# Performance work log

Hardware: AMD Instinct MI355X
Metric: run time of the kernel (lower is better)

## Reference

```python
import jax, jax.numpy as jnp
import numpy as np

MARGIN = 0.1
NUM_BINS = 1600  # FastAP histogram bins over squared-distance range [0, 4]


def _fastap_rewards(x, labels):
    """Per-query FastAP (Cakir et al.) with soft (triangular) histogram binning.
    x: [n, d] L2-normalized embeddings; labels: [n] int. Returns [n] rewards.
    Uses the fact that a triangular pulse of width delta spreads each distance
    over exactly two adjacent bins -> scatter-add instead of an [n,n,L] tensor."""
    n = x.shape[0]
    L = NUM_BINS + 1
    delta = 4.0 / NUM_BINS
    dist2 = jnp.clip(2.0 - 2.0 * (x @ x.T), 0.0, 4.0)  # [n, n]
    same = labels[:, None] == labels[None, :]
    eye = jnp.eye(n, dtype=bool)
    i_pos = same & ~eye
    i_neg = ~same

    t = dist2 / delta
    idx0 = jnp.clip(jnp.floor(t).astype(jnp.int32), 0, L - 1)
    idx1 = jnp.clip(idx0 + 1, 0, L - 1)
    frac = t - jnp.floor(t)
    rows = jnp.broadcast_to(jnp.arange(n)[:, None], (n, n))

    def hist(mask):
        m = mask.astype(x.dtype)
        h = jnp.zeros((n, L), x.dtype)
        h = h.at[rows, idx0].add((1.0 - frac) * m)
        h = h.at[rows, idx1].add(frac * m)
        return h

    h_pos = hist(i_pos)
    h_neg = hist(i_neg)
    H_pos = jnp.cumsum(h_pos, axis=1)
    H_all = jnp.cumsum(h_pos + h_neg, axis=1)
    n_pos = jnp.sum(i_pos, axis=1).astype(x.dtype)
    safe = H_all > 0
    ap = jnp.sum(jnp.where(safe, h_pos * H_pos / jnp.where(safe, H_all, 1.0), 0.0), axis=1)
    return jnp.where(n_pos > 0, ap / jnp.maximum(n_pos, 1.0), 0.0)


def _per_row_loss(inputs_col, targets_col, inputs_row, targets_row):
    """Vectorized form of compute_loss_list. Sorting in the original only serves
    to extract max pos / max neg similarity, so per-row maxima + masked sums
    reproduce the exact same math."""
    n = inputs_col.shape[0]
    sim = inputs_col @ inputs_row.T  # [n, m]
    pos = targets_col[:, None] == targets_row[None, :]
    neg = ~pos  # computed BEFORE removing the diagonal, as in the original
    eye = jnp.eye(n, dtype=bool)
    pos = pos.at[:, :n].set(pos[:, :n] & ~eye)

    has_pos = jnp.any(pos, axis=1)
    neg_max = jnp.max(jnp.where(neg, sim, -jnp.inf), axis=1)  # neg_pair_[-1]
    pos_max = jnp.max(jnp.where(pos, sim, -jnp.inf), axis=1)  # pos_pair_[-1]

    pos_sel = pos & (sim < (neg_max + MARGIN)[:, None])
    pos_loss = jnp.sum(jnp.where(pos_sel, 1.0 - sim, 0.0), axis=1)

    thr = jnp.maximum(0.6, pos_max) - MARGIN
    neg_sel = neg & (sim > thr[:, None])
    neg_loss = jnp.sum(jnp.where(neg_sel, sim, 0.0), axis=1)

    return jnp.where(has_pos, pos_loss + neg_loss, 0.0), n


def setup_inputs() -> dict:
    key = jax.random.key(0)
    k1, k2, k3, k4, k5 = jax.random.split(key, 5)
    n, m, d, ncls = 4096, 4096, 128, 512

    def unit(k, shape):
        v = jax.random.normal(k, shape, dtype=jnp.float32)
        return v / jnp.linalg.norm(v, axis=-1, keepdims=True)

    return {
        "inputs_col": unit(k1, (n, d)),
        "targets_col": jax.random.randint(k2, (n,), 0, ncls),
        "inputs_row": unit(k3, (m, d)),
        "targets_row": jax.random.randint(k4, (m,), 0, ncls),
        "reward_labels": jax.random.randint(k5, (n,), 0, ncls),
    }


def reference(inputs_col, targets_col, inputs_row, targets_row, reward_labels):
    loss_i, n = _per_row_loss(inputs_col, targets_col, inputs_row, targets_row)
    # torch.tensor(rewards) detaches rewards from the graph -> stop_gradient
    rewards = jax.lax.stop_gradient(_fastap_rewards(inputs_col, reward_labels))
    return jnp.sum(loss_i * (1.0 - rewards)) / n
```

## Files before the change

kernel.cpp:

```cpp
#include <hip/hip_runtime.h>


#define N_ROWS 4096
#define DIM 128
#define TILE 128
#define L_BINS 1601
#define WSCALE 65536.0f

typedef __bf16 bf16x8 __attribute__((ext_vector_type(8)));
typedef float f32x4 __attribute__((ext_vector_type(4)));

__device__ __forceinline__ unsigned short f32_to_bf16(float f) {
    unsigned int u = __float_as_uint(f);
    u = (u + 0x7FFFu + ((u >> 16) & 1u)) >> 16;
    return (unsigned short)u;
}

__device__ __forceinline__ float bf16_lo(unsigned int u) {
    return __uint_as_float(u << 16);
}
__device__ __forceinline__ float bf16_hi(unsigned int u) {
    return __uint_as_float(u & 0xFFFF0000u);
}

__device__ __forceinline__ void async_copy16(const void* g, void* l) {
    __builtin_amdgcn_global_load_lds(
        (const __attribute__((address_space(1))) unsigned int*)g,
        (__attribute__((address_space(3))) unsigned int*)l, 16, 0, 0);
}

__global__ __launch_bounds__(256) void cvt_bf16_kernel(const float* __restrict__ in,
                                                       unsigned short* __restrict__ out,
                                                       int count) {
    for (int idx = blockIdx.x * 256 + threadIdx.x; idx < count; idx += gridDim.x * 256)
        out[idx] = f32_to_bf16(in[idx]);
}

__global__ __launch_bounds__(256) void gemm_tile_kernel(const unsigned short* __restrict__ A,
                                                        const unsigned short* __restrict__ B,
                                                        unsigned short* __restrict__ C,
                                                        int N) {
    __shared__ unsigned short As[TILE * DIM];
    __shared__ unsigned short Bs[TILE * DIM];
    int w = threadIdx.x >> 6;
    int lane = threadIdx.x & 63;
    int tm = blockIdx.y, tn = blockIdx.x;

    const char* ga = (const char*)(A + (size_t)tm * TILE * DIM);
    const char* gb = (const char*)(B + (size_t)tn * TILE * DIM);
#pragma unroll
    for (int it = 0; it < 8; ++it) {
        int off = (w * 8 + it) * 1024;
        async_copy16(ga + off + lane * 16, (char*)As + off);
        async_copy16(gb + off + lane * 16, (char*)Bs + off);
    }
    __syncthreads();

    int wm = (w & 1) * 64;
    int wn = (w >> 1) * 64;
    int quad = lane >> 4;
    int l15 = lane & 15;

    f32x4 acc[4][4] = {};
#pragma unroll
    for (int kk = 0; kk < 4; ++kk) {
        int kb = kk * 32 + quad * 8;
        bf16x8 af[4], bfr[4];
#pragma unroll
        for (int mi = 0; mi < 4; ++mi)
            af[mi] = *(const bf16x8*)&As[(wm + mi * 16 + l15) * DIM + kb];
#pragma unroll
        for (int ni = 0; ni < 4; ++ni)
            bfr[ni] = *(const bf16x8*)&Bs[(wn + ni * 16 + l15) * DIM + kb];
#pragma unroll
        for (int mi = 0; mi < 4; ++mi)
#pragma unroll
            for (int ni = 0; ni < 4; ++ni)
                acc[mi][ni] = __builtin_amdgcn_mfma_f32_16x16x32_bf16(af[mi], bfr[ni], acc[mi][ni], 0, 0, 0);
    }

#pragma unroll
    for (int mi = 0; mi < 4; ++mi) {
        int row0 = tm * TILE + wm + mi * 16 + quad * 4;
#pragma unroll
        for (int ni = 0; ni < 4; ++ni) {
            int col = tn * TILE + wn + ni * 16 + l15;
#pragma unroll
            for (int r = 0; r < 4; ++r)
                C[(size_t)(row0 + r) * N + col] = f32_to_bf16(acc[mi][ni][r]);
        }
    }
}

__global__ __launch_bounds__(256) void loss_kernel(const unsigned short* __restrict__ sim,
                                                   const int* __restrict__ tcol,
                                                   const int* __restrict__ trow,
                                                   float* __restrict__ loss,
                                                   int n, int m) {
    __shared__ float ssim[N_ROWS];
    __shared__ char smask[N_ROWS];
    __shared__ float r1[256], r2[256];
    const float NEG_INF = -__builtin_huge_valf();
    int i = blockIdx.x;
    int t = threadIdx.x;
    int myt = tcol[i];

    const uint4* simv = (const uint4*)(sim + (size_t)i * m);
    const int4* labv = (const int4*)trow;

    float pmax = NEG_INF, nmax = NEG_INF;
    for (int v = t; v < (m >> 3); v += 256) {
        uint4 pk = simv[v];
        int4 l0 = labv[v * 2];
        int4 l1 = labv[v * 2 + 1];
        int j0 = v << 3;
        float s[8];
        s[0] = bf16_lo(pk.x); s[1] = bf16_hi(pk.x);
        s[2] = bf16_lo(pk.y); s[3] = bf16_hi(pk.y);
        s[4] = bf16_lo(pk.z); s[5] = bf16_hi(pk.z);
        s[6] = bf16_lo(pk.w); s[7] = bf16_hi(pk.w);
        int lab[8] = {l0.x, l0.y, l0.z, l0.w, l1.x, l1.y, l1.z, l1.w};
#pragma unroll
        for (int k = 0; k < 8; ++k) {
            int j = j0 + k;
            bool same = (lab[k] == myt);
            ssim[j] = s[k];
            smask[j] = same ? 1 : 0;
            if (same) {
                if (j != i && s[k] > pmax) pmax = s[k];
            } else {
                if (s[k] > nmax) nmax = s[k];
            }
        }
    }
    r1[t] = pmax; r2[t] = nmax;
    __syncthreads();
    for (int off = 128; off > 0; off >>= 1) {
        if (t < off) { r1[t] = fmaxf(r1[t], r1[t + off]); r2[t] = fmaxf(r2[t], r2[t + off]); }
        __syncthreads();
    }
    float pm = r1[0], nm = r2[0];
    __syncthreads();

    float thr_n = nm + 0.1f;
    float thr_p = fmaxf(0.6f, pm) - 0.1f;
    float pl = 0.f, nl = 0.f;
    for (int j = t; j < m; j += 256) {
        float s = ssim[j];
        if (smask[j]) {
            if (j != i && s < thr_n) pl += 1.f - s;
        } else {
            if (s > thr_p) nl += s;
        }
    }
    r1[t] = pl; r2[t] = nl;
    __syncthreads();
    for (int off = 128; off > 0; off >>= 1) {
        if (t < off) { r1[t] += r1[t + off]; r2[t] += r2[t + off]; }
        __syncthreads();
    }
    if (t == 0) loss[i] = (pm > NEG_INF) ? (r1[0] + r2[0]) : 0.f;
}

__global__ __launch_bounds__(256) void fastap_kernel(const unsigned short* __restrict__ gram,
                                                     const int* __restrict__ labels,
                                                     float* __restrict__ reward,
                                                     int n) {
    __shared__ unsigned int h_pos[L_BINS];
    __shared__ unsigned int h_all[L_BINS];
    __shared__ unsigned int sp[256], sa[256];
    __shared__ float fr[256];
    __shared__ int ir[256];
    int i = blockIdx.x;
    int t = threadIdx.x;

    for (int b = t; b < L_BINS; b += 256) { h_pos[b] = 0u; h_all[b] = 0u; }
    __syncthreads();

    int li = labels[i];
    int npos = 0;
    const uint4* gv = (const uint4*)(gram + (size_t)i * n);
    const int4* labv = (const int4*)labels;

    for (int v = t; v < (n >> 3); v += 256) {
        uint4 pk = gv[v];
        int4 l0 = labv[v * 2];
        int4 l1 = labv[v * 2 + 1];
        int j0 = v << 3;
        float s[8];
        s[0] = bf16_lo(pk.x); s[1] = bf16_hi(pk.x);
        s[2] = bf16_lo(pk.y); s[3] = bf16_hi(pk.y);
        s[4] = bf16_lo(pk.z); s[5] = bf16_hi(pk.z);
        s[6] = bf16_lo(pk.w); s[7] = bf16_hi(pk.w);
        int lab[8] = {l0.x, l0.y, l0.z, l0.w, l1.x, l1.y, l1.z, l1.w};
#pragma unroll
        for (int k = 0; k < 8; ++k) {
            int j = j0 + k;
            if (j == i) continue;
            float d2 = fminf(fmaxf(2.f - 2.f * s[k], 0.f), 4.f);
            float tt = d2 * 400.0f;
            float fl = floorf(tt);
            int i0 = (int)fl;
            if (i0 > L_BINS - 1) i0 = L_BINS - 1;
            int i1 = i0 + 1;
            if (i1 > L_BINS - 1) i1 = L_BINS - 1;
            unsigned int w1 = (unsigned int)((tt - fl) * WSCALE);
            unsigned int w0 = 65536u - w1;
            atomicAdd(&h_all[i0], w0);
            atomicAdd(&h_all[i1], w1);
            if (lab[k] == li) {
                atomicAdd(&h_pos[i0], w0);
                atomicAdd(&h_pos[i1], w1);
                npos++;
            }
        }
    }
    __syncthreads();

    const int CH = 7;
    int base = t * CH;
    unsigned int lp[CH], la[CH];
    unsigned int cp = 0u, ca = 0u;
    for (int k = 0; k < CH; ++k) {
        int idx = base + k;
        unsigned int hp = (idx < L_BINS) ? h_pos[idx] : 0u;
        unsigned int ha = (idx < L_BINS) ? h_all[idx] : 0u;
        cp += hp; ca += ha;
        lp[k] = cp; la[k] = ca;
    }
    sp[t] = cp; sa[t] = ca;
    __syncthreads();
    for (int off = 1; off < 256; off <<= 1) {
        unsigned int vp = 0u, va = 0u;
        if (t >= off) { vp = sp[t - off]; va = sa[t - off]; }
        __syncthreads();
        sp[t] += vp; sa[t] += va;
        __syncthreads();
    }
    unsigned int offp = sp[t] - cp, offa = sa[t] - ca;
    __syncthreads();

    float ap = 0.f;
    for (int k = 0; k < CH; ++k) {
        int idx = base + k;
        if (idx < L_BINS) {
            unsigned int hp = h_pos[idx];
            unsigned int Ha = la[k] + offa;
            if (hp > 0u && Ha > 0u) {
                float Hp = (float)(lp[k] + offp);
                ap += (float)hp * Hp / (float)Ha;
            }
        }
    }
    fr[t] = ap; ir[t] = npos;
    __syncthreads();
    for (int off = 128; off > 0; off >>= 1) {
        if (t < off) { fr[t] += fr[t + off]; ir[t] += ir[t + off]; }
        __syncthreads();
    }
    if (t == 0) {
        float np_ = (float)ir[0];
        reward[i] = (np_ > 0.f) ? fr[0] * (1.0f / WSCALE) / fmaxf(np_, 1.f) : 0.f;
    }
}

__global__ __launch_bounds__(256) void final_kernel(const float* __restrict__ loss,
                                                    const float* __restrict__ reward,
                                                    float* __restrict__ out, int n) {
    __shared__ float r[256];
    int t = threadIdx.x;
    float s = 0.f;
    for (int j = t; j < n; j += 256) s += loss[j] * (1.f - reward[j]);
    r[t] = s;
    __syncthreads();
    for (int off = 128; off > 0; off >>= 1) {
        if (t < off) r[t] += r[t + off];
        __syncthreads();
    }
    if (t == 0) out[0] = r[0] / (float)n;
}

extern "C" void kernel_launch(void* const* d_in, const int* in_sizes, int n_in,
                              void* d_out, int out_size, void* d_ws, size_t ws_size,
                              hipStream_t stream) {
    const float* inputs_col = (const float*)d_in[0];
    const int* targets_col = (const int*)d_in[1];
    const float* inputs_row = (const float*)d_in[2];
    const int* targets_row = (const int*)d_in[3];
    const int* reward_labels = (const int*)d_in[4];
    float* out = (float*)d_out;

    const int n = N_ROWS, m = N_ROWS, d = DIM;
    char* ws = (char*)d_ws;
    unsigned short* simbuf = (unsigned short*)ws;
    unsigned short* Abf = (unsigned short*)(ws + (size_t)33554432);
    unsigned short* Rbf = (unsigned short*)(ws + (size_t)33554432 + 1048576);
    float* loss = (float*)(ws + (size_t)33554432 + 2 * 1048576);
    float* reward = loss + n;

    cvt_bf16_kernel<<<2048, 256, 0, stream>>>(inputs_col, Abf, n * d);
    cvt_bf16_kernel<<<2048, 256, 0, stream>>>(inputs_row, Rbf, m * d);

    dim3 ggrid(n / TILE, n / TILE);
    gemm_tile_kernel<<<ggrid, 256, 0, stream>>>(Abf, Rbf, simbuf, m);

    loss_kernel<<<n, 256, 0, stream>>>(simbuf, targets_col, targets_row, loss, n, m);

    gemm_tile_kernel<<<ggrid, 256, 0, stream>>>(Abf, Abf, simbuf, n);

    fastap_kernel<<<n, 256, 0, stream>>>(simbuf, reward_labels, reward, n);

    final_kernel<<<1, 256, 0, stream>>>(loss, reward, out, n);
}
```

Measured before the change: 150.7 us.

## Merge conversions and GEMMs, use wave-per-row loss and packed 64-bit histogram

Fuses the two bf16 conversion launches into one vectorized kernel and runs both GEMMs in a single launch via a z grid dimension, writing to separate buffers. The loss kernel now uses one wavefront per row, keeps the data in registers and reduces with shuffles instead of shared memory and block barriers. The FastAP kernel packs the positive and all-pairs histograms into one 64-bit shared atomic per bin, which halves the atomics, and uses wave shuffles for the scan and reductions. The cost is a second 32MB similarity buffer and 64-bit LDS atomics.

```diff
diff --git a/kernel.cpp b/kernel.cpp
--- a/kernel.cpp
+++ b/kernel.cpp
@@ -5,7 +5,6 @@
 #define DIM 128
 #define TILE 128
 #define L_BINS 1601
-#define WSCALE 65536.0f
 
 typedef __bf16 bf16x8 __attribute__((ext_vector_type(8)));
 typedef float f32x4 __attribute__((ext_vector_type(4)));
@@ -23,28 +22,48 @@
     return __uint_as_float(u & 0xFFFF0000u);
 }
 
+__device__ __forceinline__ void unpack8(uint4 pk, float* s) {
+    s[0] = bf16_lo(pk.x); s[1] = bf16_hi(pk.x);
+    s[2] = bf16_lo(pk.y); s[3] = bf16_hi(pk.y);
+    s[4] = bf16_lo(pk.z); s[5] = bf16_hi(pk.z);
+    s[6] = bf16_lo(pk.w); s[7] = bf16_hi(pk.w);
+}
+
 __device__ __forceinline__ void async_copy16(const void* g, void* l) {
     __builtin_amdgcn_global_load_lds(
         (const __attribute__((address_space(1))) unsigned int*)g,
         (__attribute__((address_space(3))) unsigned int*)l, 16, 0, 0);
 }
 
-__global__ __launch_bounds__(256) void cvt_bf16_kernel(const float* __restrict__ in,
-                                                       unsigned short* __restrict__ out,
-                                                       int count) {
-    for (int idx = blockIdx.x * 256 + threadIdx.x; idx < count; idx += gridDim.x * 256)
-        out[idx] = f32_to_bf16(in[idx]);
+__global__ __launch_bounds__(256) void cvt2_kernel(const float4* __restrict__ a,
+                                                   const float4* __restrict__ b,
+                                                   ushort4* __restrict__ oa,
+                                                   ushort4* __restrict__ ob,
+                                                   int nvec) {
+    for (int idx = blockIdx.x * 256 + threadIdx.x; idx < 2 * nvec; idx += gridDim.x * 256) {
+        bool second = idx >= nvec;
+        int k = second ? idx - nvec : idx;
+        float4 v = second ? b[k] : a[k];
+        ushort4 o;
+        o.x = f32_to_bf16(v.x); o.y = f32_to_bf16(v.y);
+        o.z = f32_to_bf16(v.z); o.w = f32_to_bf16(v.w);
+        if (second) ob[k] = o; else oa[k] = o;
+    }
 }
 
 __global__ __launch_bounds__(256) void gemm_tile_kernel(const unsigned short* __restrict__ A,
-                                                        const unsigned short* __restrict__ B,
-                                                        unsigned short* __restrict__ C,
+                                                        const unsigned short* __restrict__ B0,
+                                                        const unsigned short* __restrict__ B1,
+                                                        unsigned short* __restrict__ C0,
+                                                        unsigned short* __restrict__ C1,
                                                         int N) {
     __shared__ unsigned short As[TILE * DIM];
     __shared__ unsigned short Bs[TILE * DIM];
     int w = threadIdx.x >> 6;
     int lane = threadIdx.x & 63;
     int tm = blockIdx.y, tn = blockIdx.x;
+    const unsigned short* B = blockIdx.z ? B1 : B0;
+    unsigned short* C = blockIdx.z ? C1 : C0;
 
     const char* ga = (const char*)(A + (size_t)tm * TILE * DIM);
     const char* gb = (const char*)(B + (size_t)tn * TILE * DIM);
@@ -97,84 +116,79 @@
                                                    const int* __restrict__ trow,
                                                    float* __restrict__ loss,
                                                    int n, int m) {
-    __shared__ float ssim[N_ROWS];
-    __shared__ char smask[N_ROWS];
-    __shared__ float r1[256], r2[256];
-    const float NEG_INF = -__builtin_huge_valf();
-    int i = blockIdx.x;
-    int t = threadIdx.x;
+    int i = (blockIdx.x * 256 + threadIdx.x) >> 6;
+    int lane = threadIdx.x & 63;
     int myt = tcol[i];
 
     const uint4* simv = (const uint4*)(sim + (size_t)i * m);
     const int4* labv = (const int4*)trow;
 
-    float pmax = NEG_INF, nmax = NEG_INF;
-    for (int v = t; v < (m >> 3); v += 256) {
-        uint4 pk = simv[v];
-        int4 l0 = labv[v * 2];
-        int4 l1 = labv[v * 2 + 1];
-        int j0 = v << 3;
+    uint4 pk[8];
+    unsigned long long posm = 0ull, negm = 0ull;
+    float pmax = -3e38f, nmax = -3e38f;
+#pragma unroll
+    for (int v = 0; v < 8; ++v) {
+        int vi = v * 64 + lane;
+        pk[v] = simv[vi];
+        int4 l0 = labv[2 * vi];
+        int4 l1 = labv[2 * vi + 1];
+        int j0 = vi * 8;
         float s[8];
-        s[0] = bf16_lo(pk.x); s[1] = bf16_hi(pk.x);
-        s[2] = bf16_lo(pk.y); s[3] = bf16_hi(pk.y);
-        s[4] = bf16_lo(pk.z); s[5] = bf16_hi(pk.z);
-        s[6] = bf16_lo(pk.w); s[7] = bf16_hi(pk.w);
+        unpack8(pk[v], s);
         int lab[8] = {l0.x, l0.y, l0.z, l0.w, l1.x, l1.y, l1.z, l1.w};
 #pragma unroll
         for (int k = 0; k < 8; ++k) {
             int j = j0 + k;
             bool same = (lab[k] == myt);
-            ssim[j] = s[k];
-            smask[j] = same ? 1 : 0;
-            if (same) {
-                if (j != i && s[k] > pmax) pmax = s[k];
-            } else {
-                if (s[k] > nmax) nmax = s[k];
-            }
-        }
-    }
-    r1[t] = pmax; r2[t] = nmax;
-    __syncthreads();
-    for (int off = 128; off > 0; off >>= 1) {
-        if (t < off) { r1[t] = fmaxf(r1[t], r1[t + off]); r2[t] = fmaxf(r2[t], r2[t + off]); }
-        __syncthreads();
-    }
-    float pm = r1[0], nm = r2[0];
-    __syncthreads();
-
-    float thr_n = nm + 0.1f;
-    float thr_p = fmaxf(0.6f, pm) - 0.1f;
+            bool posf = same && (j != i);
+            if (posf) pmax = fmaxf(pmax, s[k]);
+            if (!same) nmax = fmaxf(nmax, s[k]);
+            posm |= ((unsigned long long)posf) << (v * 8 + k);
+            negm |= ((unsigned long long)(!same)) << (v * 8 + k);
+        }
+    }
+#pragma unroll
+    for (int off = 32; off > 0; off >>= 1) {
+        pmax = fmaxf(pmax, __shfl_xor(pmax, off));
+        nmax = fmaxf(nmax, __shfl_xor(nmax, off));
+    }
+
+    float thr_n = nmax + 0.1f;
+    float thr_p = fmaxf(0.6f, pmax) - 0.1f;
     float pl = 0.f, nl = 0.f;
-    for (int j = t; j < m; j += 256) {
-        float s = ssim[j];
-        if (smask[j]) {
-            if (j != i && s < thr_n) pl += 1.f - s;
-        } else {
-            if (s > thr_p) nl += s;
-        }
-    }
-    r1[t] = pl; r2[t] = nl;
-    __syncthreads();
-    for (int off = 128; off > 0; off >>= 1) {
-        if (t < off) { r1[t] += r1[t + off]; r2[t] += r2[t + off]; }
-        __syncthreads();
-    }
-    if (t == 0) loss[i] = (pm > NEG_INF) ? (r1[0] + r2[0]) : 0.f;
+#pragma unroll
+    for (int v = 0; v < 8; ++v) {
+        float s[8];
+        unpack8(pk[v], s);
+#pragma unroll
+        for (int k = 0; k < 8; ++k) {
+            int bit = v * 8 + k;
+            bool posf = (posm >> bit) & 1ull;
+            bool negf = (negm >> bit) & 1ull;
+            pl += (posf && s[k] < thr_n) ? 1.f - s[k] : 0.f;
+            nl += (negf && s[k] > thr_p) ? s[k] : 0.f;
+        }
+    }
+    float tot = pl + nl;
+#pragma unroll
+    for (int off = 32; off > 0; off >>= 1) tot += __shfl_xor(tot, off);
+    if (lane == 0) loss[i] = (pmax > -1e30f) ? tot : 0.f;
 }
 
 __global__ __launch_bounds__(256) void fastap_kernel(const unsigned short* __restrict__ gram,
                                                      const int* __restrict__ labels,
                                                      float* __restrict__ reward,
                                                      int n) {
-    __shared__ unsigned int h_pos[L_BINS];
-    __shared__ unsigned int h_all[L_BINS];
-    __shared__ unsigned int sp[256], sa[256];
-    __shared__ float fr[256];
-    __shared__ int ir[256];
+    __shared__ unsigned long long hist[L_BINS];
+    __shared__ unsigned long long wsum[4];
+    __shared__ float apw[4];
+    __shared__ int npw[4];
     int i = blockIdx.x;
     int t = threadIdx.x;
-
-    for (int b = t; b < L_BINS; b += 256) { h_pos[b] = 0u; h_all[b] = 0u; }
+    int w = t >> 6;
+    int lane = t & 63;
+
+    for (int b = t; b < L_BINS; b += 256) hist[b] = 0ull;
     __syncthreads();
 
     int li = labels[i];
@@ -184,19 +198,15 @@
 
     for (int v = t; v < (n >> 3); v += 256) {
         uint4 pk = gv[v];
-        int4 l0 = labv[v * 2];
-        int4 l1 = labv[v * 2 + 1];
+        int4 l0 = labv[2 * v];
+        int4 l1 = labv[2 * v + 1];
         int j0 = v << 3;
         float s[8];
-        s[0] = bf16_lo(pk.x); s[1] = bf16_hi(pk.x);
-        s[2] = bf16_lo(pk.y); s[3] = bf16_hi(pk.y);
-        s[4] = bf16_lo(pk.z); s[5] = bf16_hi(pk.z);
-        s[6] = bf16_lo(pk.w); s[7] = bf16_hi(pk.w);
+        unpack8(pk, s);
         int lab[8] = {l0.x, l0.y, l0.z, l0.w, l1.x, l1.y, l1.z, l1.w};
 #pragma unroll
         for (int k = 0; k < 8; ++k) {
             int j = j0 + k;
-            if (j == i) continue;
             float d2 = fminf(fmaxf(2.f - 2.f * s[k], 0.f), 4.f);
             float tt = d2 * 400.0f;
             float fl = floorf(tt);
@@ -204,63 +214,69 @@
             if (i0 > L_BINS - 1) i0 = L_BINS - 1;
             int i1 = i0 + 1;
             if (i1 > L_BINS - 1) i1 = L_BINS - 1;
-            unsigned int w1 = (unsigned int)((tt - fl) * WSCALE);
+            unsigned int w1 = (unsigned int)((tt - fl) * 65536.0f);
             unsigned int w0 = 65536u - w1;
-            atomicAdd(&h_all[i0], w0);
-            atomicAdd(&h_all[i1], w1);
-            if (lab[k] == li) {
-                atomicAdd(&h_pos[i0], w0);
-                atomicAdd(&h_pos[i1], w1);
-                npos++;
-            }
+            bool diag = (j == i);
+            if (diag) { w0 = 0u; w1 = 0u; }
+            bool posf = (lab[k] == li) && !diag;
+            unsigned long long hi = posf ? 1ull : 0ull;
+            atomicAdd(&hist[i0], (unsigned long long)w0 | ((hi * w0) << 32));
+            atomicAdd(&hist[i1], (unsigned long long)w1 | ((hi * w1) << 32));
+            npos += posf ? 1 : 0;
         }
     }
     __syncthreads();
 
     const int CH = 7;
     int base = t * CH;
-    unsigned int lp[CH], la[CH];
-    unsigned int cp = 0u, ca = 0u;
+    unsigned long long lc[CH];
+    unsigned long long run = 0ull;
+#pragma unroll
     for (int k = 0; k < CH; ++k) {
         int idx = base + k;
-        unsigned int hp = (idx < L_BINS) ? h_pos[idx] : 0u;
-        unsigned int ha = (idx < L_BINS) ? h_all[idx] : 0u;
-        cp += hp; ca += ha;
-        lp[k] = cp; la[k] = ca;
-    }
-    sp[t] = cp; sa[t] = ca;
-    __syncthreads();
-    for (int off = 1; off < 256; off <<= 1) {
-        unsigned int vp = 0u, va = 0u;
-        if (t >= off) { vp = sp[t - off]; va = sa[t - off]; }
-        __syncthreads();
-        sp[t] += vp; sa[t] += va;
-        __syncthreads();
-    }
-    unsigned int offp = sp[t] - cp, offa = sa[t] - ca;
-    __syncthreads();
+        unsigned long long h = (idx < L_BINS) ? hist[idx] : 0ull;
+        run += h;
+        lc[k] = run;
+    }
+    unsigned long long tsum = run;
+    unsigned long long sc = tsum;
+#pragma unroll
+    for (int off = 1; off < 64; off <<= 1) {
+        unsigned long long v2 = __shfl_up(sc, off);
+        if (lane >= off) sc += v2;
+    }
+    if (lane == 63) wsum[w] = sc;
+    __syncthreads();
+    unsigned long long woff = 0ull;
+    for (int ww = 0; ww < w; ++ww) woff += wsum[ww];
+    unsigned long long throff = woff + sc - tsum;
 
     float ap = 0.f;
+#pragma unroll
     for (int k = 0; k < CH; ++k) {
         int idx = base + k;
         if (idx < L_BINS) {
-            unsigned int hp = h_pos[idx];
-            unsigned int Ha = la[k] + offa;
-            if (hp > 0u && Ha > 0u) {
-                float Hp = (float)(lp[k] + offp);
-                ap += (float)hp * Hp / (float)Ha;
+            unsigned long long h = hist[idx];
+            unsigned int hp = (unsigned int)(h >> 32);
+            if (hp) {
+                unsigned long long cum = lc[k] + throff;
+                unsigned int Hp = (unsigned int)(cum >> 32);
+                unsigned int Ha = (unsigned int)cum;
+                ap += (float)hp * (float)Hp / (float)Ha;
             }
         }
     }
-    fr[t] = ap; ir[t] = npos;
-    __syncthreads();
-    for (int off = 128; off > 0; off >>= 1) {
-        if (t < off) { fr[t] += fr[t + off]; ir[t] += ir[t + off]; }
-        __syncthreads();
-    }
+#pragma unroll
+    for (int off = 32; off > 0; off >>= 1) {
+        ap += __shfl_xor(ap, off);
+        npos += __shfl_xor(npos, off);
+    }
+    if (lane == 0) { apw[w] = ap; npw[w] = npos; }
+    __syncthreads();
     if (t == 0) {
-        float np_ = (float)ir[0];
-        reward[i] = (np_ > 0.f) ? fr[0] * (1.0f / WSCALE) / fmaxf(np_, 1.f) : 0.f;
+        float A = apw[0] + apw[1] + apw[2] + apw[3];
+        int np = npw[0] + npw[1] + npw[2] + npw[3];
+        reward[i] = (np > 0) ? A * (1.0f / 65536.0f) / (float)np : 0.f;
     }
 }
 
@@ -292,23 +308,23 @@
 
     const int n = N_ROWS, m = N_ROWS, d = DIM;
     char* ws = (char*)d_ws;
+    const size_t MB = 1048576;
     unsigned short* simbuf = (unsigned short*)ws;
-    unsigned short* Abf = (unsigned short*)(ws + (size_t)33554432);
-    unsigned short* Rbf = (unsigned short*)(ws + (size_t)33554432 + 1048576);
-    float* loss = (float*)(ws + (size_t)33554432 + 2 * 1048576);
+    unsigned short* grambuf = (unsigned short*)(ws + 32 * MB);
+    unsigned short* Abf = (unsigned short*)(ws + 64 * MB);
+    unsigned short* Rbf = (unsigned short*)(ws + 65 * MB);
+    float* loss = (float*)(ws + 66 * MB);
     float* reward = loss + n;
 
-    cvt_bf16_kernel<<<2048, 256, 0, stream>>>(inputs_col, Abf, n * d);
-    cvt_bf16_kernel<<<2048, 256, 0, stream>>>(inputs_row, Rbf, m * d);
-
-    dim3 ggrid(n / TILE, n / TILE);
-    gemm_tile_kernel<<<ggrid, 256, 0, stream>>>(Abf, Rbf, simbuf, m);
-
-    loss_kernel<<<n, 256, 0, stream>>>(simbuf, targets_col, targets_row, loss, n, m);
-
-    gemm_tile_kernel<<<ggrid, 256, 0, stream>>>(Abf, Abf, simbuf, n);
-
-    fastap_kernel<<<n, 256, 0, stream>>>(simbuf, reward_labels, reward, n);
+    cvt2_kernel<<<512, 256, 0, stream>>>((const float4*)inputs_col, (const float4*)inputs_row,
+                                         (ushort4*)Abf, (ushort4*)Rbf, n * d / 4);
+
+    dim3 ggrid(n / TILE, n / TILE, 2);
+    gemm_tile_kernel<<<ggrid, 256, 0, stream>>>(Abf, Rbf, Abf, simbuf, grambuf, m);
+
+    loss_kernel<<<n / 4, 256, 0, stream>>>(simbuf, targets_col, targets_row, loss, n, m);
+
+    fastap_kernel<<<n, 256, 0, stream>>>(grambuf, reward_labels, reward, n);
 
     final_kernel<<<1, 256, 0, stream>>>(loss, reward, out, n);
 }
```

Result: faster. 135.8 us (-9.9%).
